# Kernel tuning notes

Hardware: AMD Instinct MI355X
Metric: run time of the kernel (lower is better)

## Reference

```python
import jax, jax.numpy as jnp
import numpy as np

C = 128
GROUPS = 8
EPS = 1e-5


def setup_inputs() -> dict:
    key = jax.random.key(0)
    ks = jax.random.split(key, 7)
    x = jax.random.normal(ks[0], (8, C, 256, 256), dtype=jnp.float32)
    gn_w = jax.random.normal(ks[1], (C,), dtype=jnp.float32) * 0.02 + 1.0
    gn_b = jax.random.normal(ks[2], (C,), dtype=jnp.float32) * 0.02
    w1 = jax.random.normal(ks[3], (C, C), dtype=jnp.float32) * (1.0 / np.sqrt(C))
    b1 = jax.random.normal(ks[4], (C,), dtype=jnp.float32) * 0.02
    w2 = jax.random.normal(ks[5], (C, C), dtype=jnp.float32) * (1.0 / np.sqrt(C))
    b2 = jax.random.normal(ks[6], (C,), dtype=jnp.float32) * 0.02
    return {"x": x, "gn_w": gn_w, "gn_b": gn_b, "w1": w1, "b1": b1, "w2": w2, "b2": b2}


def reference(x, gn_w, gn_b, w1, b1, w2, b2):
    # fft2 -> ifft2(..).real round-trip (faithful to original; numerically ~identity)
    x_ifft = jnp.fft.ifft2(jnp.fft.fft2(x, axes=(-2, -1)), axes=(-2, -1)).real.astype(x.dtype)

    # GroupNorm over (C//G, H, W) per group
    B, Ch, H, W = x_ifft.shape
    g = x_ifft.reshape(B, GROUPS, Ch // GROUPS, H, W)
    mean = g.mean(axis=(2, 3, 4), keepdims=True)
    var = g.var(axis=(2, 3, 4), keepdims=True)
    xn = ((g - mean) * jax.lax.rsqrt(var + EPS)).reshape(B, Ch, H, W)
    xn = xn * gn_w[None, :, None, None] + gn_b[None, :, None, None]

    # 1x1 conv -> ReLU -> 1x1 conv (as channel GEMMs)
    h = jnp.einsum('oc,bchw->bohw', w1, xn) + b1[None, :, None, None]
    h = jax.nn.relu(h)
    ffn = jnp.einsum('oc,bchw->bohw', w2, h) + b2[None, :, None, None]
    return x_ifft + ffn
```

## Files before the change

### kernel.cpp

```cpp
#include <hip/hip_runtime.h>

typedef __attribute__((ext_vector_type(8))) short s16x8;
typedef __attribute__((ext_vector_type(4))) float f32x4;

#define CCH 128

__device__ __forceinline__ ushort f2bf(float f) {
  uint u = __float_as_uint(f);
  u += 0x7fffu + ((u >> 16) & 1u);
  return (ushort)(u >> 16);
}
__device__ __forceinline__ float bf2f(ushort u) {
  return __uint_as_float(((uint)u) << 16);
}

__device__ __forceinline__ int swz(int row, int col) {
  return (row << 7) | (col ^ ((row & 7) << 3));
}

__global__ __launch_bounds__(256) void pass1_stats_tr(const float* __restrict__ x,
                                                      ushort* __restrict__ xb,
                                                      float2* __restrict__ partials) {
  __shared__ ushort sT[256 * CCH];
  __shared__ float ws1[4][8], ws2[4][8];
  const int t = threadIdx.x;
  const int b = blockIdx.x >> 8;
  const int p0 = (blockIdx.x & 255) << 8;
  const int wv = t >> 6, lane = t & 63;
  const int px4 = lane << 2;
  float sg1[8], sg2[8];
#pragma unroll
  for (int g = 0; g < 8; ++g) { sg1[g] = 0.f; sg2[g] = 0.f; }

  const float* xbase = x + (((size_t)b * CCH) << 16) + p0;
#pragma unroll
  for (int i = 0; i < 8; ++i) {
    const int ch = i * 16 + wv * 4;
    float4 v[4];
#pragma unroll
    for (int j = 0; j < 4; ++j)
      v[j] = *(const float4*)(xbase + (((size_t)(ch + j)) << 16) + px4);
#pragma unroll
    for (int j = 0; j < 4; ++j) {
      sg1[i] += v[j].x + v[j].y + v[j].z + v[j].w;
      sg2[i] += v[j].x * v[j].x + v[j].y * v[j].y + v[j].z * v[j].z + v[j].w * v[j].w;
    }
#pragma unroll
    for (int k = 0; k < 4; ++k) {
      const int row = px4 + k;
      const int gs = (i * 4 + wv) ^ (((row >> 3) & 15) << 1);
      ushort4 pk;
      pk.x = f2bf(((const float*)&v[0])[k]);
      pk.y = f2bf(((const float*)&v[1])[k]);
      pk.z = f2bf(((const float*)&v[2])[k]);
      pk.w = f2bf(((const float*)&v[3])[k]);
      *(ushort4*)&sT[row * CCH + gs * 4] = pk;
    }
  }
#pragma unroll
  for (int g = 0; g < 8; ++g) {
    float a = sg1[g], q = sg2[g];
#pragma unroll
    for (int off = 32; off > 0; off >>= 1) {
      a += __shfl_down(a, off);
      q += __shfl_down(q, off);
    }
    if (lane == 0) { ws1[wv][g] = a; ws2[wv][g] = q; }
  }
  __syncthreads();
  if (t < 8) {
    float a = ws1[0][t] + ws1[1][t] + ws1[2][t] + ws1[3][t];
    float q = ws2[0][t] + ws2[1][t] + ws2[2][t] + ws2[3][t];
    partials[blockIdx.x * 8 + t] = (float2){a, q};
  }
  const int c16 = t & 15, pr = t >> 4;
  ushort* dst = xb + ((size_t)((b << 16) + p0)) * CCH;
#pragma unroll
  for (int s = 0; s < 16; ++s) {
    const int row = s * 16 + pr;
    const int gs = (c16 * 2) ^ (((row >> 3) & 15) << 1);
    *(s16x8*)&dst[(size_t)row * CCH + c16 * 8] = *(const s16x8*)&sT[row * CCH + gs * 4];
  }
}

__global__ void stats_finalize2(const float2* __restrict__ partials,
                                const float* __restrict__ gn_w,
                                const float* __restrict__ gn_b,
                                float* __restrict__ scale, float* __restrict__ shift) {
  const int t = threadIdx.x;
  const int b = t >> 3, g = t & 7;
  float s1 = 0.f, s2 = 0.f;
  for (int c = 0; c < 256; ++c) {
    float2 p = partials[(b * 256 + c) * 8 + g];
    s1 += p.x;
    s2 += p.y;
  }
  const float invN = 1.0f / 1048576.0f;
  const float mean = s1 * invN;
  const float var = s2 * invN - mean * mean;
  const float rstd = rsqrtf(var + 1e-5f);
  for (int i = 0; i < 16; ++i) {
    const int c = g * 16 + i;
    const float sc = rstd * gn_w[c];
    scale[b * CCH + c] = sc;
    shift[b * CCH + c] = gn_b[c] - mean * sc;
  }
}

__global__ __launch_bounds__(256) void prep_w2(const float* __restrict__ w2,
                                               ushort* __restrict__ w2b) {
  int i = blockIdx.x * 256 + threadIdx.x;
  float4 a = ((const float4*)w2)[i];
  ushort4 o;
  o.x = f2bf(a.x); o.y = f2bf(a.y); o.z = f2bf(a.z); o.w = f2bf(a.w);
  ((ushort4*)w2b)[i] = o;
}

__global__ __launch_bounds__(128) void fold_w1(const float* __restrict__ w1,
                                               const float* __restrict__ b1,
                                               const float* __restrict__ scale,
                                               const float* __restrict__ shift,
                                               ushort* __restrict__ W1b,
                                               float* __restrict__ c1) {
  const int b = blockIdx.x >> 7, o = blockIdx.x & 127, c = threadIdx.x;
  const float wv = w1[o * CCH + c];
  W1b[(b << 14) + o * CCH + c] = f2bf(wv * scale[b * CCH + c]);
  float s = wv * shift[b * CCH + c];
#pragma unroll
  for (int off = 32; off > 0; off >>= 1) s += __shfl_down(s, off);
  __shared__ float tmp[2];
  if ((threadIdx.x & 63) == 0) tmp[threadIdx.x >> 6] = s;
  __syncthreads();
  if (threadIdx.x == 0) c1[(b << 7) + o] = tmp[0] + tmp[1] + b1[o];
}

__global__ __launch_bounds__(256, 4) void mlp_tiled(
    const ushort* __restrict__ xb, const ushort* __restrict__ W1b,
    const ushort* __restrict__ w2b, const float* __restrict__ c1,
    const float* __restrict__ b2, float* __restrict__ out) {
  __shared__ ushort sB[128 * CCH];
  float* sF = (float*)sB;
  const int t = threadIdx.x;
  const int b = blockIdx.x >> 9;
  const int p0 = (blockIdx.x & 511) << 7;
  const int lane = t & 63;
  const int wv = t >> 6;
  const int fl = lane & 15;
  const int fh = lane >> 4;

  const ushort* src = xb + ((size_t)((b << 16) + p0)) * CCH;
#pragma unroll
  for (int i = 0; i < 8; ++i) {
    const int u = i * 256 + t;
    const int px = u >> 4;
    const int ch = (u & 15) * 8;
    const s16x8 v = *(const s16x8*)(src + px * CCH + ch);
    *(s16x8*)&sB[swz(px, ch)] = v;
  }
  __syncthreads();

  f32x4 acc[2][8];
#pragma unroll
  for (int f = 0; f < 2; ++f)
#pragma unroll
    for (int j = 0; j < 8; ++j) acc[f][j] = (f32x4){0.f, 0.f, 0.f, 0.f};

  const ushort* w1p = W1b + (b << 14);
#pragma unroll
  for (int k0 = 0; k0 < 128; k0 += 32) {
    const int kb = k0 + fh * 8;
    const s16x8 a0 = *(const s16x8*)(w1p + (wv * 32 + fl) * CCH + kb);
    const s16x8 a1 = *(const s16x8*)(w1p + (wv * 32 + 16 + fl) * CCH + kb);
#pragma unroll
    for (int j = 0; j < 8; ++j) {
      const s16x8 bf = *(const s16x8*)&sB[swz(j * 16 + fl, kb)];
      acc[0][j] = __builtin_amdgcn_mfma_f32_16x16x32_bf16(a0, bf, acc[0][j], 0, 0, 0);
      acc[1][j] = __builtin_amdgcn_mfma_f32_16x16x32_bf16(a1, bf, acc[1][j], 0, 0, 0);
    }
  }
  __syncthreads();

  const float* c1b = c1 + (b << 7);
#pragma unroll
  for (int f = 0; f < 2; ++f) {
    const int ob = wv * 32 + f * 16 + fh * 4;
    const float4 cc = *(const float4*)(c1b + ob);
#pragma unroll
    for (int j = 0; j < 8; ++j) {
      ushort4 pk;
      pk.x = f2bf(fmaxf(acc[f][j][0] + cc.x, 0.f));
      pk.y = f2bf(fmaxf(acc[f][j][1] + cc.y, 0.f));
      pk.z = f2bf(fmaxf(acc[f][j][2] + cc.z, 0.f));
      pk.w = f2bf(fmaxf(acc[f][j][3] + cc.w, 0.f));
      *(ushort4*)&sB[swz(j * 16 + fl, ob)] = pk;
    }
  }
  __syncthreads();

  f32x4 acc2[2][8];
#pragma unroll
  for (int f = 0; f < 2; ++f)
#pragma unroll
    for (int j = 0; j < 8; ++j) acc2[f][j] = (f32x4){0.f, 0.f, 0.f, 0.f};

#pragma unroll
  for (int k0 = 0; k0 < 128; k0 += 32) {
    const int kb = k0 + fh * 8;
    const s16x8 a0 = *(const s16x8*)(w2b + (wv * 32 + fl) * CCH + kb);
    const s16x8 a1 = *(const s16x8*)(w2b + (wv * 32 + 16 + fl) * CCH + kb);
#pragma unroll
    for (int j = 0; j < 8; ++j) {
      const s16x8 bf = *(const s16x8*)&sB[swz(j * 16 + fl, kb)];
      acc2[0][j] = __builtin_amdgcn_mfma_f32_16x16x32_bf16(a0, bf, acc2[0][j], 0, 0, 0);
      acc2[1][j] = __builtin_amdgcn_mfma_f32_16x16x32_bf16(a1, bf, acc2[1][j], 0, 0, 0);
    }
  }
  __syncthreads();

  const int rowbase = wv * 16;
#pragma unroll
  for (int f = 0; f < 2; ++f) {
    const int ob = wv * 32 + f * 16 + fh * 4;
    const float4 bb = *(const float4*)(b2 + ob);
    ushort4 rx[8];
#pragma unroll
    for (int j = 0; j < 8; ++j)
      rx[j] = *(const ushort4*)(src + (j * 16 + fl) * CCH + ob);
#pragma unroll
    for (int j = 0; j < 8; ++j) {
      const int px = j * 16 + fl;
      const int rb = (rowbase + fh * 4) * 128 + px;
      sF[rb]       = acc2[f][j][0] + bb.x + bf2f(rx[j].x);
      sF[rb + 128] = acc2[f][j][1] + bb.y + bf2f(rx[j].y);
      sF[rb + 256] = acc2[f][j][2] + bb.z + bf2f(rx[j].z);
      sF[rb + 384] = acc2[f][j][3] + bb.w + bf2f(rx[j].w);
    }
#pragma unroll
    for (int i = 0; i < 16; ++i) {
      const float2 v = *(const float2*)&sF[(rowbase + i) * 128 + lane * 2];
      const int ch = wv * 32 + f * 16 + i;
      *(float2*)(out + (((size_t)(b * CCH + ch)) << 16) + p0 + lane * 2) = v;
    }
  }
}

extern "C" void kernel_launch(void* const* d_in, const int* in_sizes, int n_in,
                              void* d_out, int out_size, void* d_ws, size_t ws_size,
                              hipStream_t stream) {
  const float* x    = (const float*)d_in[0];
  const float* gn_w = (const float*)d_in[1];
  const float* gn_b = (const float*)d_in[2];
  const float* w1   = (const float*)d_in[3];
  const float* b1   = (const float*)d_in[4];
  const float* w2   = (const float*)d_in[5];
  const float* b2   = (const float*)d_in[6];
  float* out = (float*)d_out;
  char* ws = (char*)d_ws;

  const size_t XB_BYTES = (size_t)8 * 65536 * CCH * 2;
  ushort* xbuf  = (ushort*)ws;
  float2* parts = (float2*)(ws + XB_BYTES);
  float* scale  = (float*)(ws + XB_BYTES + 131072);
  float* shift  = (float*)(ws + XB_BYTES + 135168);
  ushort* w2b   = (ushort*)(ws + XB_BYTES + 139264);
  ushort* W1b   = (ushort*)(ws + XB_BYTES + 172032);
  float* c1     = (float*)(ws + XB_BYTES + 434176);

  hipLaunchKernelGGL(pass1_stats_tr, dim3(2048), dim3(256), 0, stream, x, xbuf, parts);
  hipLaunchKernelGGL(prep_w2, dim3(16), dim3(256), 0, stream, w2, w2b);
  hipLaunchKernelGGL(stats_finalize2, dim3(1), dim3(64), 0, stream, parts, gn_w, gn_b, scale, shift);
  hipLaunchKernelGGL(fold_w1, dim3(1024), dim3(128), 0, stream, w1, b1, scale, shift, W1b, c1);
  hipLaunchKernelGGL(mlp_tiled, dim3(4096), dim3(256), 0, stream, xbuf, W1b, w2b, c1, b2, out);
}
```

Measured before the change: 218.1 us.

## Make MLP kernel persistent with double-buffered async LDS loads of tiles

The MLP kernel becomes a persistent loop over eight pixel tiles per block. Each next tile is prefetched into a second LDS buffer with global_load_lds while the current tile goes through both GEMMs, so global reads overlap with MFMA work. The residual is now read from LDS before the tile is overwritten, and xb is stored pre-swizzled so the direct LDS copy lands in the layout the GEMM expects. pass1 moves to 128-pixel tiles with an XCD-aware block remap, and workspace regions are overlapped (partials share space with W1b). In exchange, the MLP grid shrinks to 512 blocks and uses more LDS per block, which lowers occupancy.

```diff
diff --git a/kernel.cpp b/kernel.cpp
--- a/kernel.cpp
+++ b/kernel.cpp
@@ -2,6 +2,7 @@
 
 typedef __attribute__((ext_vector_type(8))) short s16x8;
 typedef __attribute__((ext_vector_type(4))) float f32x4;
+typedef unsigned int u32;
 
 #define CCH 128
 
@@ -18,37 +19,46 @@
   return (row << 7) | (col ^ ((row & 7) << 3));
 }
 
-__global__ __launch_bounds__(256) void pass1_stats_tr(const float* __restrict__ x,
-                                                      ushort* __restrict__ xb,
-                                                      float2* __restrict__ partials) {
-  __shared__ ushort sT[256 * CCH];
-  __shared__ float ws1[4][8], ws2[4][8];
+__device__ __forceinline__ void gll16(const void* g, void* l) {
+  __builtin_amdgcn_global_load_lds((const __attribute__((address_space(1))) u32*)g,
+                                   (__attribute__((address_space(3))) u32*)l, 16, 0, 0);
+}
+
+__global__ __launch_bounds__(256) void pass1(const float* __restrict__ x,
+                                             ushort* __restrict__ xb,
+                                             float2* __restrict__ partials) {
+  __shared__ ushort sT[128 * CCH];
+  __shared__ float wsa[4][4], wsb[4][4];
   const int t = threadIdx.x;
-  const int b = blockIdx.x >> 8;
-  const int p0 = (blockIdx.x & 255) << 8;
+  const int blk = ((blockIdx.x & 7) << 9) | (blockIdx.x >> 3);
+  const int b = blk >> 9;
+  const int p0 = (blk & 511) << 7;
   const int wv = t >> 6, lane = t & 63;
-  const int px4 = lane << 2;
-  float sg1[8], sg2[8];
-#pragma unroll
-  for (int g = 0; g < 8; ++g) { sg1[g] = 0.f; sg2[g] = 0.f; }
+  const int px4 = (t & 31) * 4;
+  const int c8 = t >> 5;
+
+  float sa[4], sq[4];
+#pragma unroll
+  for (int i = 0; i < 4; ++i) { sa[i] = 0.f; sq[i] = 0.f; }
 
   const float* xbase = x + (((size_t)b * CCH) << 16) + p0;
 #pragma unroll
-  for (int i = 0; i < 8; ++i) {
-    const int ch = i * 16 + wv * 4;
+  for (int i = 0; i < 4; ++i) {
+    const int ch = i * 32 + c8 * 4;
     float4 v[4];
 #pragma unroll
     for (int j = 0; j < 4; ++j)
       v[j] = *(const float4*)(xbase + (((size_t)(ch + j)) << 16) + px4);
 #pragma unroll
     for (int j = 0; j < 4; ++j) {
-      sg1[i] += v[j].x + v[j].y + v[j].z + v[j].w;
-      sg2[i] += v[j].x * v[j].x + v[j].y * v[j].y + v[j].z * v[j].z + v[j].w * v[j].w;
-    }
+      sa[i] += v[j].x + v[j].y + v[j].z + v[j].w;
+      sq[i] += v[j].x * v[j].x + v[j].y * v[j].y + v[j].z * v[j].z + v[j].w * v[j].w;
+    }
+    const int c4 = i * 8 + c8;
 #pragma unroll
     for (int k = 0; k < 4; ++k) {
       const int row = px4 + k;
-      const int gs = (i * 4 + wv) ^ (((row >> 3) & 15) << 1);
+      const int gs = c4 ^ (((row >> 3) & 15) << 1);
       ushort4 pk;
       pk.x = f2bf(((const float*)&v[0])[k]);
       pk.y = f2bf(((const float*)&v[1])[k]);
@@ -58,28 +68,30 @@
     }
   }
 #pragma unroll
-  for (int g = 0; g < 8; ++g) {
-    float a = sg1[g], q = sg2[g];
+  for (int i = 0; i < 4; ++i) {
+    float a = sa[i], q = sq[i];
 #pragma unroll
     for (int off = 32; off > 0; off >>= 1) {
       a += __shfl_down(a, off);
       q += __shfl_down(q, off);
     }
-    if (lane == 0) { ws1[wv][g] = a; ws2[wv][g] = q; }
+    if (lane == 0) { wsa[wv][i] = a; wsb[wv][i] = q; }
   }
   __syncthreads();
   if (t < 8) {
-    float a = ws1[0][t] + ws1[1][t] + ws1[2][t] + ws1[3][t];
-    float q = ws2[0][t] + ws2[1][t] + ws2[2][t] + ws2[3][t];
-    partials[blockIdx.x * 8 + t] = (float2){a, q};
-  }
-  const int c16 = t & 15, pr = t >> 4;
-  ushort* dst = xb + ((size_t)((b << 16) + p0)) * CCH;
-#pragma unroll
-  for (int s = 0; s < 16; ++s) {
+    const int g = t;
+    const int w0 = (g & 1) * 2, ii = g >> 1;
+    partials[blk * 8 + g] =
+        (float2){wsa[w0][ii] + wsa[w0 + 1][ii], wsb[w0][ii] + wsb[w0 + 1][ii]};
+  }
+  const int g = t & 15, pr = t >> 4;
+  ushort* dst = xb + ((size_t)blk << 14);
+#pragma unroll
+  for (int s = 0; s < 8; ++s) {
     const int row = s * 16 + pr;
-    const int gs = (c16 * 2) ^ (((row >> 3) & 15) << 1);
-    *(s16x8*)&dst[(size_t)row * CCH + c16 * 8] = *(const s16x8*)&sT[row * CCH + gs * 4];
+    const int sidx = row * CCH + (((2 * g) ^ (((row >> 3) & 15) << 1)) * 4);
+    const int didx = row * CCH + ((g ^ (row & 7)) * 8);
+    *(s16x8*)&dst[didx] = *(const s16x8*)&sT[sidx];
   }
 }
 
@@ -90,8 +102,8 @@
   const int t = threadIdx.x;
   const int b = t >> 3, g = t & 7;
   float s1 = 0.f, s2 = 0.f;
-  for (int c = 0; c < 256; ++c) {
-    float2 p = partials[(b * 256 + c) * 8 + g];
+  for (int c = 0; c < 512; ++c) {
+    float2 p = partials[(b * 512 + c) * 8 + g];
     s1 += p.x;
     s2 += p.y;
   }
@@ -134,113 +146,139 @@
   if (threadIdx.x == 0) c1[(b << 7) + o] = tmp[0] + tmp[1] + b1[o];
 }
 
-__global__ __launch_bounds__(256, 4) void mlp_tiled(
+#define NT 8
+__global__ __launch_bounds__(256) void mlp_pipe(
     const ushort* __restrict__ xb, const ushort* __restrict__ W1b,
     const ushort* __restrict__ w2b, const float* __restrict__ c1,
     const float* __restrict__ b2, float* __restrict__ out) {
-  __shared__ ushort sB[128 * CCH];
-  float* sF = (float*)sB;
-  const int t = threadIdx.x;
-  const int b = blockIdx.x >> 9;
-  const int p0 = (blockIdx.x & 511) << 7;
-  const int lane = t & 63;
-  const int wv = t >> 6;
-  const int fl = lane & 15;
-  const int fh = lane >> 4;
-
-  const ushort* src = xb + ((size_t)((b << 16) + p0)) * CCH;
-#pragma unroll
-  for (int i = 0; i < 8; ++i) {
-    const int u = i * 256 + t;
-    const int px = u >> 4;
-    const int ch = (u & 15) * 8;
-    const s16x8 v = *(const s16x8*)(src + px * CCH + ch);
-    *(s16x8*)&sB[swz(px, ch)] = v;
-  }
-  __syncthreads();
-
-  f32x4 acc[2][8];
-#pragma unroll
-  for (int f = 0; f < 2; ++f)
-#pragma unroll
-    for (int j = 0; j < 8; ++j) acc[f][j] = (f32x4){0.f, 0.f, 0.f, 0.f};
-
+  __shared__ ushort sB[2][128 * CCH];
+  const int t = threadIdx.x, lane = t & 63, wv = t >> 6;
+  const int fl = lane & 15, fh = lane >> 4;
+  const int blk = ((blockIdx.x & 7) << 6) | (blockIdx.x >> 3);
+  const int gt0 = blk * NT;
+  const int b = gt0 >> 9;
   const ushort* w1p = W1b + (b << 14);
-#pragma unroll
-  for (int k0 = 0; k0 < 128; k0 += 32) {
-    const int kb = k0 + fh * 8;
-    const s16x8 a0 = *(const s16x8*)(w1p + (wv * 32 + fl) * CCH + kb);
-    const s16x8 a1 = *(const s16x8*)(w1p + (wv * 32 + 16 + fl) * CCH + kb);
-#pragma unroll
-    for (int j = 0; j < 8; ++j) {
-      const s16x8 bf = *(const s16x8*)&sB[swz(j * 16 + fl, kb)];
-      acc[0][j] = __builtin_amdgcn_mfma_f32_16x16x32_bf16(a0, bf, acc[0][j], 0, 0, 0);
-      acc[1][j] = __builtin_amdgcn_mfma_f32_16x16x32_bf16(a1, bf, acc[1][j], 0, 0, 0);
-    }
-  }
-  __syncthreads();
-
   const float* c1b = c1 + (b << 7);
-#pragma unroll
-  for (int f = 0; f < 2; ++f) {
-    const int ob = wv * 32 + f * 16 + fh * 4;
-    const float4 cc = *(const float4*)(c1b + ob);
-#pragma unroll
-    for (int j = 0; j < 8; ++j) {
-      ushort4 pk;
-      pk.x = f2bf(fmaxf(acc[f][j][0] + cc.x, 0.f));
-      pk.y = f2bf(fmaxf(acc[f][j][1] + cc.y, 0.f));
-      pk.z = f2bf(fmaxf(acc[f][j][2] + cc.z, 0.f));
-      pk.w = f2bf(fmaxf(acc[f][j][3] + cc.w, 0.f));
-      *(ushort4*)&sB[swz(j * 16 + fl, ob)] = pk;
-    }
-  }
-  __syncthreads();
-
-  f32x4 acc2[2][8];
-#pragma unroll
-  for (int f = 0; f < 2; ++f)
-#pragma unroll
-    for (int j = 0; j < 8; ++j) acc2[f][j] = (f32x4){0.f, 0.f, 0.f, 0.f};
-
-#pragma unroll
-  for (int k0 = 0; k0 < 128; k0 += 32) {
-    const int kb = k0 + fh * 8;
-    const s16x8 a0 = *(const s16x8*)(w2b + (wv * 32 + fl) * CCH + kb);
-    const s16x8 a1 = *(const s16x8*)(w2b + (wv * 32 + 16 + fl) * CCH + kb);
-#pragma unroll
-    for (int j = 0; j < 8; ++j) {
-      const s16x8 bf = *(const s16x8*)&sB[swz(j * 16 + fl, kb)];
-      acc2[0][j] = __builtin_amdgcn_mfma_f32_16x16x32_bf16(a0, bf, acc2[0][j], 0, 0, 0);
-      acc2[1][j] = __builtin_amdgcn_mfma_f32_16x16x32_bf16(a1, bf, acc2[1][j], 0, 0, 0);
-    }
-  }
-  __syncthreads();
-
-  const int rowbase = wv * 16;
-#pragma unroll
-  for (int f = 0; f < 2; ++f) {
-    const int ob = wv * 32 + f * 16 + fh * 4;
-    const float4 bb = *(const float4*)(b2 + ob);
-    ushort4 rx[8];
-#pragma unroll
-    for (int j = 0; j < 8; ++j)
-      rx[j] = *(const ushort4*)(src + (j * 16 + fl) * CCH + ob);
-#pragma unroll
-    for (int j = 0; j < 8; ++j) {
-      const int px = j * 16 + fl;
-      const int rb = (rowbase + fh * 4) * 128 + px;
-      sF[rb]       = acc2[f][j][0] + bb.x + bf2f(rx[j].x);
-      sF[rb + 128] = acc2[f][j][1] + bb.y + bf2f(rx[j].y);
-      sF[rb + 256] = acc2[f][j][2] + bb.z + bf2f(rx[j].z);
-      sF[rb + 384] = acc2[f][j][3] + bb.w + bf2f(rx[j].w);
-    }
-#pragma unroll
-    for (int i = 0; i < 16; ++i) {
-      const float2 v = *(const float2*)&sF[(rowbase + i) * 128 + lane * 2];
-      const int ch = wv * 32 + f * 16 + i;
-      *(float2*)(out + (((size_t)(b * CCH + ch)) << 16) + p0 + lane * 2) = v;
-    }
+
+  {
+    const char* s0 = (const char*)xb + ((size_t)gt0 << 15) + wv * 8192 + lane * 16;
+    ushort* l0 = &sB[0][wv * 4096];
+#pragma unroll
+    for (int i = 0; i < 8; ++i) gll16(s0 + i * 1024, l0 + i * 512);
+  }
+
+#pragma unroll 1
+  for (int it = 0; it < NT; ++it) {
+    const int cur = it & 1;
+    const int gt = gt0 + it;
+    if (it + 1 < NT) {
+      const char* s0 = (const char*)xb + ((size_t)(gt + 1) << 15) + wv * 8192 + lane * 16;
+      ushort* l0 = &sB[cur ^ 1][wv * 4096];
+#pragma unroll
+      for (int i = 0; i < 8; ++i) gll16(s0 + i * 1024, l0 + i * 512);
+      __builtin_amdgcn_sched_barrier(0);
+      asm volatile("s_waitcnt vmcnt(8)" ::: "memory");
+    } else {
+      asm volatile("s_waitcnt vmcnt(0)" ::: "memory");
+    }
+    __builtin_amdgcn_sched_barrier(0);
+    __builtin_amdgcn_s_barrier();
+    __builtin_amdgcn_sched_barrier(0);
+
+    ushort* sb = &sB[cur][0];
+
+    f32x4 acc[2][8];
+#pragma unroll
+    for (int f = 0; f < 2; ++f)
+#pragma unroll
+      for (int j = 0; j < 8; ++j) acc[f][j] = (f32x4){0.f, 0.f, 0.f, 0.f};
+#pragma unroll
+    for (int k0 = 0; k0 < 128; k0 += 32) {
+      const int kb = k0 + fh * 8;
+      const s16x8 a0 = *(const s16x8*)(w1p + (wv * 32 + fl) * CCH + kb);
+      const s16x8 a1 = *(const s16x8*)(w1p + (wv * 32 + 16 + fl) * CCH + kb);
+#pragma unroll
+      for (int j = 0; j < 8; ++j) {
+        const s16x8 bf = *(const s16x8*)&sb[swz(j * 16 + fl, kb)];
+        acc[0][j] = __builtin_amdgcn_mfma_f32_16x16x32_bf16(a0, bf, acc[0][j], 0, 0, 0);
+        acc[1][j] = __builtin_amdgcn_mfma_f32_16x16x32_bf16(a1, bf, acc[1][j], 0, 0, 0);
+      }
+    }
+    asm volatile("s_waitcnt lgkmcnt(0)" ::: "memory");
+    __builtin_amdgcn_sched_barrier(0);
+    __builtin_amdgcn_s_barrier();
+    __builtin_amdgcn_sched_barrier(0);
+
+    ushort4 rx[2][8];
+#pragma unroll
+    for (int f = 0; f < 2; ++f) {
+      const int ob = wv * 32 + f * 16 + fh * 4;
+      const float4 cc = *(const float4*)(c1b + ob);
+#pragma unroll
+      for (int j = 0; j < 8; ++j) {
+        ushort* p = &sb[swz(j * 16 + fl, ob)];
+        rx[f][j] = *(const ushort4*)p;
+        ushort4 pk;
+        pk.x = f2bf(fmaxf(acc[f][j][0] + cc.x, 0.f));
+        pk.y = f2bf(fmaxf(acc[f][j][1] + cc.y, 0.f));
+        pk.z = f2bf(fmaxf(acc[f][j][2] + cc.z, 0.f));
+        pk.w = f2bf(fmaxf(acc[f][j][3] + cc.w, 0.f));
+        *(ushort4*)p = pk;
+      }
+    }
+    asm volatile("s_waitcnt lgkmcnt(0)" ::: "memory");
+    __builtin_amdgcn_sched_barrier(0);
+    __builtin_amdgcn_s_barrier();
+    __builtin_amdgcn_sched_barrier(0);
+
+    f32x4 acc2[2][8];
+#pragma unroll
+    for (int f = 0; f < 2; ++f)
+#pragma unroll
+      for (int j = 0; j < 8; ++j) acc2[f][j] = (f32x4){0.f, 0.f, 0.f, 0.f};
+#pragma unroll
+    for (int k0 = 0; k0 < 128; k0 += 32) {
+      const int kb = k0 + fh * 8;
+      const s16x8 a0 = *(const s16x8*)(w2b + (wv * 32 + fl) * CCH + kb);
+      const s16x8 a1 = *(const s16x8*)(w2b + (wv * 32 + 16 + fl) * CCH + kb);
+#pragma unroll
+      for (int j = 0; j < 8; ++j) {
+        const s16x8 bf = *(const s16x8*)&sb[swz(j * 16 + fl, kb)];
+        acc2[0][j] = __builtin_amdgcn_mfma_f32_16x16x32_bf16(a0, bf, acc2[0][j], 0, 0, 0);
+        acc2[1][j] = __builtin_amdgcn_mfma_f32_16x16x32_bf16(a1, bf, acc2[1][j], 0, 0, 0);
+      }
+    }
+    asm volatile("s_waitcnt lgkmcnt(0)" ::: "memory");
+    __builtin_amdgcn_sched_barrier(0);
+    __builtin_amdgcn_s_barrier();
+    __builtin_amdgcn_sched_barrier(0);
+
+    float* sF = (float*)sb;
+    const int p0 = (gt & 511) << 7;
+    const int rowbase = wv * 16;
+#pragma unroll
+    for (int f = 0; f < 2; ++f) {
+      const int ob = wv * 32 + f * 16 + fh * 4;
+      const float4 bb = *(const float4*)(b2 + ob);
+#pragma unroll
+      for (int j = 0; j < 8; ++j) {
+        const int rb = (rowbase + fh * 4) * 128 + j * 16 + fl;
+        sF[rb]       = acc2[f][j][0] + bb.x + bf2f(rx[f][j].x);
+        sF[rb + 128] = acc2[f][j][1] + bb.y + bf2f(rx[f][j].y);
+        sF[rb + 256] = acc2[f][j][2] + bb.z + bf2f(rx[f][j].z);
+        sF[rb + 384] = acc2[f][j][3] + bb.w + bf2f(rx[f][j].w);
+      }
+#pragma unroll
+      for (int i = 0; i < 16; ++i) {
+        const float2 v = *(const float2*)&sF[(rowbase + i) * 128 + lane * 2];
+        const int ch = wv * 32 + f * 16 + i;
+        *(float2*)(out + (((size_t)(b * CCH + ch)) << 16) + p0 + lane * 2) = v;
+      }
+    }
+    asm volatile("s_waitcnt lgkmcnt(0)" ::: "memory");
+    __builtin_amdgcn_sched_barrier(0);
+    __builtin_amdgcn_s_barrier();
+    __builtin_amdgcn_sched_barrier(0);
   }
 }
 
@@ -257,18 +295,18 @@
   float* out = (float*)d_out;
   char* ws = (char*)d_ws;
 
-  const size_t XB_BYTES = (size_t)8 * 65536 * CCH * 2;
+  const size_t XB = (size_t)8 * 65536 * CCH * 2;
   ushort* xbuf  = (ushort*)ws;
-  float2* parts = (float2*)(ws + XB_BYTES);
-  float* scale  = (float*)(ws + XB_BYTES + 131072);
-  float* shift  = (float*)(ws + XB_BYTES + 135168);
-  ushort* w2b   = (ushort*)(ws + XB_BYTES + 139264);
-  ushort* W1b   = (ushort*)(ws + XB_BYTES + 172032);
-  float* c1     = (float*)(ws + XB_BYTES + 434176);
-
-  hipLaunchKernelGGL(pass1_stats_tr, dim3(2048), dim3(256), 0, stream, x, xbuf, parts);
-  hipLaunchKernelGGL(prep_w2, dim3(16), dim3(256), 0, stream, w2, w2b);
+  float2* parts = (float2*)(ws + XB);
+  ushort* W1b   = (ushort*)(ws + XB);
+  float* scale  = (float*)(ws + XB + 262144);
+  float* shift  = (float*)(ws + XB + 266240);
+  ushort* w2b   = (ushort*)(ws + XB + 270336);
+  float* c1     = (float*)(ws + XB + 303104);
+
+  hipLaunchKernelGGL(pass1, dim3(4096), dim3(256), 0, stream, x, xbuf, parts);
   hipLaunchKernelGGL(stats_finalize2, dim3(1), dim3(64), 0, stream, parts, gn_w, gn_b, scale, shift);
   hipLaunchKernelGGL(fold_w1, dim3(1024), dim3(128), 0, stream, w1, b1, scale, shift, W1b, c1);
-  hipLaunchKernelGGL(mlp_tiled, dim3(4096), dim3(256), 0, stream, xbuf, W1b, w2b, c1, b2, out);
-}
+  hipLaunchKernelGGL(prep_w2, dim3(16), dim3(256), 0, stream, w2, w2b);
+  hipLaunchKernelGGL(mlp_pipe, dim3(512), dim3(256), 0, stream, xbuf, W1b, w2b, c1, b2, out);
+}
```

New measurement: 260.5 us. +19.4%, slower.
